# Performance work log

Hardware: AMD Instinct MI355X
Metric: run time of the kernel (lower is better)

## Reference

```python
import jax, jax.numpy as jnp
import numpy as np

N, E, NG = 4096, 8192, 256
AF, BF, H, L = 9, 4, 128, 3
LN_EPS = 1e-5


def _layernorm(x, g, b):
    mu = jnp.mean(x, axis=-1, keepdims=True)
    var = jnp.var(x, axis=-1, keepdims=True)
    return (x - mu) * jax.lax.rsqrt(var + LN_EPS) * g + b


def setup_inputs() -> dict:
    key = jax.random.key(0)
    ks = jax.random.split(key, 20)
    x = jax.random.normal(ks[0], (N, AF), dtype=jnp.float32)
    edge_index = jax.random.randint(ks[1], (2, E), 0, N, dtype=jnp.int64)
    edge_attr = jax.random.normal(ks[2], (E, BF), dtype=jnp.float32)
    batch = jnp.sort(jax.random.randint(ks[3], (N,), 0, NG, dtype=jnp.int64))
    s = lambda f: 1.0 / np.sqrt(f)
    return {
        "x": x, "edge_index": edge_index, "edge_attr": edge_attr, "batch": batch,
        "atom_w": jax.random.normal(ks[4], (AF, H), jnp.float32) * s(AF),
        "atom_b": jnp.zeros((H,), jnp.float32),
        # per-layer edge-network params, stacked over L layers
        "e1_w": jax.random.normal(ks[5], (L, BF, H), jnp.float32) * s(BF),
        "e1_b": jnp.zeros((L, H), jnp.float32),
        "e2_w": jax.random.normal(ks[6], (L, H, H * H), jnp.float32) * s(H),
        "e2_b": jnp.zeros((L, H * H), jnp.float32),
        "root_w": jax.random.normal(ks[7], (L, H, H), jnp.float32) * s(H),
        "conv_b": jnp.zeros((L, H), jnp.float32),
        "ln_g": jnp.ones((L, H), jnp.float32),
        "ln_b": jnp.zeros((L, H), jnp.float32),
        "head_w1": jax.random.normal(ks[8], (H, H // 2), jnp.float32) * s(H),
        "head_b1": jnp.zeros((H // 2,), jnp.float32),
        "head_w2": jax.random.normal(ks[9], (H // 2, 1), jnp.float32) * s(H // 2),
        "head_b2": jnp.zeros((1,), jnp.float32),
    }


def reference(x, edge_index, edge_attr, batch, atom_w, atom_b, e1_w, e1_b,
              e2_w, e2_b, root_w, conv_b, ln_g, ln_b, head_w1, head_b1,
              head_w2, head_b2):
    src, dst = edge_index[0], edge_index[1]
    h = jax.nn.relu(x @ atom_w + atom_b)  # [N, H]
    # in-degree for mean aggregation (empty -> 0 via clamp on denominator)
    deg = jax.ops.segment_sum(jnp.ones((E,), h.dtype), dst, num_segments=N)
    denom = jnp.maximum(deg, 1.0)[:, None]
    for l in range(L):
        # edge network: bond features -> per-edge HxH weight matrix
        eh = jax.nn.gelu(edge_attr @ e1_w[l] + e1_b[l], approximate=False)
        w = (eh @ e2_w[l] + e2_b[l]).reshape(E, H, H)  # [E, H, H]
        # gather source node features, per-edge matvec, scatter-mean to dst
        msg = jnp.einsum('ei,eio->eo', h[src], w)  # [E, H]
        agg = jax.ops.segment_sum(msg, dst, num_segments=N) / denom
        h_new = jax.nn.relu(agg + h @ root_w[l] + conv_b[l])
        h = _layernorm(h + h_new, ln_g[l], ln_b[l])
        # dropout: eval mode (identity)
    # global mean pool over graphs
    cnt = jnp.maximum(jax.ops.segment_sum(jnp.ones((N,), h.dtype), batch, num_segments=NG), 1.0)
    mol = jax.ops.segment_sum(h, batch, num_segments=NG) / cnt[:, None]
    hid = jax.nn.gelu(mol @ head_w1 + head_b1, approximate=False)
    logits = (hid @ head_w2 + head_b2).squeeze(-1)  # [NG]
    return logits
```

## Files before the change

kernel.cpp:

```cpp
#include <hip/hip_runtime.h>
#include <hip/hip_bf16.h>

#define N_NODES 4096
#define N_EDGES 8192
#define NGRAPH  256
#define AFEAT   9
#define BFEAT   4
#define H       128
#define NL      3
#define KS      129
#define SPLITS  4
#define TILE_E  64
#define SLICE_SH    16384
#define SLICE_BYTES 32768

typedef short short8 __attribute__((ext_vector_type(8)));
typedef float f32x4 __attribute__((ext_vector_type(4)));

__device__ __forceinline__ short f2b(float f){
    union { float f; unsigned u; } c; c.f = f;
    unsigned r = c.u + 0x7FFFu + ((c.u >> 16) & 1u);
    return (short)(r >> 16);
}
__device__ __forceinline__ float gelu_exact(float x){
    return 0.5f * x * (1.0f + erff(x * 0.70710678118654752440f));
}

__global__ void k_prep_b(const float* __restrict__ e2w, const float* __restrict__ e2b,
                         short* __restrict__ bt){
    __shared__ float ts[H][33];
    int b  = blockIdx.x;
    int o0 = (b & 3) * 32;
    int k  = (b >> 2) % KS;
    int l  = (b >> 2) / KS;
    const float* src = (k < H) ? (e2w + ((size_t)l * H + k) * (H * H))
                               : (e2b + (size_t)l * (H * H));
    for (int idx = threadIdx.x; idx < H * 32; idx += 256){
        int i = idx >> 5, op = idx & 31;
        ts[i][op] = src[i * H + o0 + op];
    }
    __syncthreads();
    short* dst = bt + (size_t)(l * KS + k) * SLICE_SH;
    for (int idx = threadIdx.x; idx < 32 * H; idx += 256){
        int j    = idx & 7;
        int quad = (idx >> 3) & 3;
        int op   = (idx >> 5) & 31;
        int ic   = idx >> 10;
        int i    = ic * 32 + quad * 8 + j;
        int o    = o0 + op;
        dst[((((o >> 4) * 4 + ic) * 64) + quad * 16 + (o & 15)) * 8 + j] = f2b(ts[i][op]);
    }
}

__global__ void k_atom(const float* __restrict__ x, const float* __restrict__ aw,
                       const float* __restrict__ ab, float* __restrict__ h,
                       short* __restrict__ hb){
    __shared__ float xs[AFEAT];
    int n = blockIdx.x, o = threadIdx.x;
    if (o < AFEAT) xs[o] = x[n * AFEAT + o];
    __syncthreads();
    float a = ab[o];
    #pragma unroll
    for (int f = 0; f < AFEAT; ++f) a += xs[f] * aw[f * H + o];
    a = fmaxf(a, 0.0f);
    h[(size_t)n * H + o]  = a;
    hb[(size_t)n * H + o] = f2b(a);
}

__global__ void k_deg(const int* __restrict__ ei, int* __restrict__ ideg){
    int e = blockIdx.x * 256 + threadIdx.x;
    if (e < N_EDGES) atomicAdd(&ideg[ei[N_EDGES + e]], 1);
}

__global__ void k_scan(const int* __restrict__ ideg, int* __restrict__ row_ptr,
                       int* __restrict__ cursor){
    __shared__ int part[256];
    int t = threadIdx.x;
    int base = t * 16;
    int loc[16]; int s = 0;
    #pragma unroll
    for (int i = 0; i < 16; ++i){ loc[i] = s; s += ideg[base + i]; }
    part[t] = s;
    __syncthreads();
    if (t == 0){
        int run = 0;
        for (int i = 0; i < 256; ++i){ int v = part[i]; part[i] = run; run += v; }
        row_ptr[N_NODES] = run;
    }
    __syncthreads();
    int off = part[t];
    #pragma unroll
    for (int i = 0; i < 16; ++i){
        row_ptr[base + i] = off + loc[i];
        cursor[base + i]  = off + loc[i];
    }
}

__global__ void k_fill(const int* __restrict__ ei, int* __restrict__ cursor,
                       int* __restrict__ eidx){
    int e = blockIdx.x * 256 + threadIdx.x;
    if (e < N_EDGES){
        int d = ei[N_EDGES + e];
        int pos = atomicAdd(&cursor[d], 1);
        eidx[pos] = e;
    }
}

__global__ void k_edge_mlp(const float* __restrict__ ea, const float* __restrict__ w1,
                           const float* __restrict__ b1, float* __restrict__ ehT){
    __shared__ float as[BFEAT];
    int e = blockIdx.x, o = threadIdx.x;
    if (o < BFEAT) as[o] = ea[e * BFEAT + o];
    __syncthreads();
    #pragma unroll
    for (int l = 0; l < NL; ++l){
        float v = b1[l * H + o];
        #pragma unroll
        for (int f = 0; f < BFEAT; ++f) v += as[f] * w1[(l * BFEAT + f) * H + o];
        v = gelu_exact(v);
        ehT[((size_t)l * KS + o) * N_EDGES + e] = v;
        if (o == 0) ehT[((size_t)l * KS + H) * N_EDGES + e] = 1.0f;
    }
}

__global__ __launch_bounds__(256, 2)
void k_msg_gemm(const short* __restrict__ bt, const float* __restrict__ ehT,
                const short* __restrict__ hb, const int* __restrict__ ei,
                float* __restrict__ parts, int l){
    __shared__ __align__(16) float ehs[33 * TILE_E];

    const int tid  = threadIdx.x;
    const int lane = tid & 63, w = tid >> 6;
    const int col  = lane & 15, quad = lane >> 4;

    const int split = blockIdx.x & 3;
    const int ohalf = (blockIdx.x >> 2) & 1;
    const int tile  = blockIdx.x >> 3;
    const int t     = ohalf * 4 + w;
    const int kbeg  = (KS * split) >> 2;
    const int kend  = (KS * (split + 1)) >> 2;
    const int kcnt  = kend - kbeg;
    const int ebase = tile * TILE_E;

    for (int idx = tid; idx < kcnt * TILE_E; idx += 256){
        int kk = idx >> 6, e = idx & 63;
        ehs[idx] = ehT[((size_t)(l * KS + kbeg + kk)) * N_EDGES + ebase + e];
    }

    short8 gf[4][4];
    #pragma unroll
    for (int m = 0; m < 4; ++m){
        int e = ebase + m * 16 + col;
        int s = ei[e];
        const char* gb = (const char*)hb + ((size_t)s * H + quad * 8) * 2;
        #pragma unroll
        for (int ic = 0; ic < 4; ++ic)
            gf[m][ic] = *(const short8*)(gb + ic * 64);
    }

    float acc[4][4];
    #pragma unroll
    for (int m = 0; m < 4; ++m)
        #pragma unroll
        for (int r = 0; r < 4; ++r) acc[m][r] = 0.0f;

    const char* bsrc = (const char*)bt + (size_t)(l * KS + kbeg) * SLICE_BYTES
                     + t * 4096 + lane * 16;

    short8 X[4], Y[4];

    auto loadB = [&](short8 (&B)[4], int kk){
        const char* p = bsrc + (size_t)kk * SLICE_BYTES;
        #pragma unroll
        for (int ic = 0; ic < 4; ++ic)
            B[ic] = *(const short8*)(p + ic * 1024);
    };
    auto computeB = [&](const short8 (&B)[4], int kk){
        __builtin_amdgcn_s_setprio(1);
        #pragma unroll
        for (int m = 0; m < 4; ++m){
            f32x4 ev = *(const f32x4*)(ehs + kk * TILE_E + m * 16 + quad * 4);
            f32x4 U = {0.0f, 0.0f, 0.0f, 0.0f};
            #pragma unroll
            for (int ic = 0; ic < 4; ++ic)
                U = __builtin_amdgcn_mfma_f32_16x16x32_bf16(gf[m][ic], B[ic], U, 0, 0, 0);
            #pragma unroll
            for (int r = 0; r < 4; ++r)
                acc[m][r] += ev[r] * U[r];
        }
        __builtin_amdgcn_s_setprio(0);
    };

    loadB(X, 0);
    __syncthreads();

    int kk = 0;
    for (; kk + 2 <= kcnt; kk += 2){
        loadB(Y, kk + 1);
        computeB(X, kk);
        if (kk + 2 < kcnt) loadB(X, kk + 2);
        computeB(Y, kk + 1);
    }
    if (kk < kcnt) computeB(X, kk);

    float* pb = parts + (size_t)split * N_EDGES * H + (size_t)ebase * H + t * 16;
    #pragma unroll
    for (int m = 0; m < 4; ++m)
        #pragma unroll
        for (int r = 0; r < 4; ++r)
            pb[(size_t)(m * 16 + quad * 4 + r) * H + col] = acc[m][r];
}

__global__ void k_node(const float* __restrict__ parts, const int* __restrict__ eidx,
                       const int* __restrict__ row_ptr,
                       const float* __restrict__ rw, const float* __restrict__ cb,
                       const float* __restrict__ lg, const float* __restrict__ lb,
                       float* __restrict__ h, short* __restrict__ hb, int l){
    __shared__ float hs[H];
    __shared__ float rsum[2], rsq[2];
    int n = blockIdx.x, o = threadIdx.x;
    float hv = h[(size_t)n * H + o];
    hs[o] = hv;
    int p0 = row_ptr[n], p1 = row_ptr[n + 1];
    float a = 0.0f;
    for (int p = p0; p < p1; ++p){
        const float* pr = parts + (size_t)eidx[p] * H + o;
        #pragma unroll
        for (int s = 0; s < SPLITS; ++s) a += pr[(size_t)s * N_EDGES * H];
    }
    int d = p1 - p0;
    a *= 1.0f / (float)(d > 0 ? d : 1);
    __syncthreads();
    float root = cb[l * H + o];
    const float* W = rw + (size_t)l * H * H;
    #pragma unroll 8
    for (int i = 0; i < H; ++i) root += hs[i] * W[i * H + o];
    float hn = fmaxf(a + root, 0.0f);
    float v  = hv + hn;
    float s = v, q = v * v;
    #pragma unroll
    for (int off = 32; off > 0; off >>= 1){
        s += __shfl_down(s, off, 64);
        q += __shfl_down(q, off, 64);
    }
    if ((o & 63) == 0){ rsum[o >> 6] = s; rsq[o >> 6] = q; }
    __syncthreads();
    float S = rsum[0] + rsum[1], Q = rsq[0] + rsq[1];
    float mean = S * (1.0f / H);
    float var  = Q * (1.0f / H) - mean * mean;
    float out  = (v - mean) * rsqrtf(var + 1e-5f) * lg[l * H + o] + lb[l * H + o];
    h[(size_t)n * H + o]  = out;
    hb[(size_t)n * H + o] = f2b(out);
}

__global__ void k_pool(const float* __restrict__ h, const int* __restrict__ batch,
                       float* __restrict__ molsum, float* __restrict__ cnt){
    int idx = blockIdx.x * 256 + threadIdx.x;
    int n = idx >> 7, o = idx & 127;
    int b = batch[n];
    atomicAdd(&molsum[b * H + o], h[idx]);
    if (o == 0) atomicAdd(&cnt[b], 1.0f);
}

__global__ void k_head(const float* __restrict__ molsum, const float* __restrict__ cnt,
                       const float* __restrict__ w1, const float* __restrict__ b1,
                       const float* __restrict__ w2, const float* __restrict__ b2,
                       float* __restrict__ out){
    __shared__ float mol[H];
    int g = blockIdx.x, t = threadIdx.x;
    float c = fmaxf(cnt[g], 1.0f);
    mol[t]      = molsum[g * H + t] / c;
    mol[t + 64] = molsum[g * H + t + 64] / c;
    __syncthreads();
    float a = b1[t];
    #pragma unroll 8
    for (int i = 0; i < H; ++i) a += mol[i] * w1[i * 64 + t];
    float hid = gelu_exact(a);
    float p = hid * w2[t];
    #pragma unroll
    for (int off = 32; off > 0; off >>= 1) p += __shfl_down(p, off, 64);
    if (t == 0) out[g] = p + b2[0];
}

extern "C" void kernel_launch(void* const* d_in, const int* in_sizes, int n_in,
                              void* d_out, int out_size, void* d_ws, size_t ws_size,
                              hipStream_t stream){
    (void)in_sizes; (void)n_in; (void)out_size; (void)ws_size;
    const float* x     = (const float*)d_in[0];
    const int*   ei    = (const int*)  d_in[1];
    const float* ea    = (const float*)d_in[2];
    const int*   batch = (const int*)  d_in[3];
    const float* aw    = (const float*)d_in[4];
    const float* ab    = (const float*)d_in[5];
    const float* e1w   = (const float*)d_in[6];
    const float* e1b   = (const float*)d_in[7];
    const float* e2w   = (const float*)d_in[8];
    const float* e2b   = (const float*)d_in[9];
    const float* rw    = (const float*)d_in[10];
    const float* cb    = (const float*)d_in[11];
    const float* lg    = (const float*)d_in[12];
    const float* lb    = (const float*)d_in[13];
    const float* hw1   = (const float*)d_in[14];
    const float* hb1   = (const float*)d_in[15];
    const float* hw2   = (const float*)d_in[16];
    const float* hb2   = (const float*)d_in[17];
    float* out = (float*)d_out;

    char* p = (char*)d_ws;
    auto carve = [&](size_t bytes){ char* r = p; p += (bytes + 255) & ~(size_t)255; return r; };
    short* bt     = (short*)carve((size_t)NL * KS * SLICE_SH * 2);
    float* h      = (float*)carve((size_t)N_NODES * H * 4);
    short* hbuf   = (short*)carve((size_t)N_NODES * H * 2);
    float* ehT    = (float*)carve((size_t)NL * KS * N_EDGES * 4);
    float* parts  = (float*)carve((size_t)SPLITS * N_EDGES * H * 4);
    int*   ideg   = (int*)  carve((size_t)N_NODES * 4);
    int*   row_ptr= (int*)  carve((size_t)(N_NODES + 1) * 4);
    int*   cursor = (int*)  carve((size_t)N_NODES * 4);
    int*   eidx   = (int*)  carve((size_t)N_EDGES * 4);
    float* molsum = (float*)carve((size_t)NGRAPH * H * 4);
    float* cnt    = (float*)carve((size_t)NGRAPH * 4);

    hipMemsetAsync(ideg, 0, (size_t)N_NODES * 4, stream);
    hipMemsetAsync(molsum, 0, (size_t)NGRAPH * H * 4, stream);
    hipMemsetAsync(cnt, 0, (size_t)NGRAPH * 4, stream);

    k_prep_b<<<NL * KS * 4, 256, 0, stream>>>(e2w, e2b, bt);
    k_atom<<<N_NODES, H, 0, stream>>>(x, aw, ab, h, hbuf);
    k_deg<<<N_EDGES / 256, 256, 0, stream>>>(ei, ideg);
    k_scan<<<1, 256, 0, stream>>>(ideg, row_ptr, cursor);
    k_fill<<<N_EDGES / 256, 256, 0, stream>>>(ei, cursor, eidx);
    k_edge_mlp<<<N_EDGES, H, 0, stream>>>(ea, e1w, e1b, ehT);

    for (int l = 0; l < NL; ++l){
        k_msg_gemm<<<(N_EDGES / TILE_E) * 2 * SPLITS, 256, 0, stream>>>(bt, ehT, hbuf, ei, parts, l);
        k_node<<<N_NODES, H, 0, stream>>>(parts, eidx, row_ptr, rw, cb, lg, lb, h, hbuf, l);
    }
    k_pool<<<N_NODES * H / 256, 256, 0, stream>>>(h, batch, molsum, cnt);
    k_head<<<NGRAPH, 64, 0, stream>>>(molsum, cnt, hw1, hb1, hw2, hb2, out);
}
```

Measured before the change: 320.5 us.

## Use three K splits with triple-buffered B loads, batch nodes, fuse pooling

The message GEMM now splits K into three equal slices of 43 instead of four uneven ones, and triple-buffers the B-fragment loads to hide more global latency. The node kernel handles four nodes per block so each root-weight load is reused across them, and the last layer folds mean pooling into it through atomics, removing the separate pool kernel. The edge MLP is relaid so each thread handles one edge for one output channel, giving coalesced ehT writes. In exchange the GEMM launches fewer blocks, uses more registers for the third buffer, and the node kernel has fewer blocks in flight.

```diff
diff --git a/kernel.cpp b/kernel.cpp
--- a/kernel.cpp
+++ b/kernel.cpp
@@ -9,8 +9,10 @@
 #define H       128
 #define NL      3
 #define KS      129
-#define SPLITS  4
+#define SPLITS  3
+#define KSPL    43
 #define TILE_E  64
+#define NPB     4
 #define SLICE_SH    16384
 #define SLICE_BYTES 32768
 
@@ -108,15 +110,16 @@
 
 __global__ void k_edge_mlp(const float* __restrict__ ea, const float* __restrict__ w1,
                            const float* __restrict__ b1, float* __restrict__ ehT){
-    __shared__ float as[BFEAT];
-    int e = blockIdx.x, o = threadIdx.x;
-    if (o < BFEAT) as[o] = ea[e * BFEAT + o];
-    __syncthreads();
+    int o = blockIdx.x >> 5;
+    int e = (blockIdx.x & 31) * 256 + threadIdx.x;
+    float4 a = *(const float4*)(ea + (size_t)e * BFEAT);
     #pragma unroll
     for (int l = 0; l < NL; ++l){
-        float v = b1[l * H + o];
-        #pragma unroll
-        for (int f = 0; f < BFEAT; ++f) v += as[f] * w1[(l * BFEAT + f) * H + o];
+        float v = b1[l * H + o]
+                + a.x * w1[(l * BFEAT + 0) * H + o]
+                + a.y * w1[(l * BFEAT + 1) * H + o]
+                + a.z * w1[(l * BFEAT + 2) * H + o]
+                + a.w * w1[(l * BFEAT + 3) * H + o];
         v = gelu_exact(v);
         ehT[((size_t)l * KS + o) * N_EDGES + e] = v;
         if (o == 0) ehT[((size_t)l * KS + H) * N_EDGES + e] = 1.0f;
@@ -127,19 +130,19 @@
 void k_msg_gemm(const short* __restrict__ bt, const float* __restrict__ ehT,
                 const short* __restrict__ hb, const int* __restrict__ ei,
                 float* __restrict__ parts, int l){
-    __shared__ __align__(16) float ehs[33 * TILE_E];
+    __shared__ __align__(16) float ehs[KSPL * TILE_E];
 
     const int tid  = threadIdx.x;
     const int lane = tid & 63, w = tid >> 6;
     const int col  = lane & 15, quad = lane >> 4;
 
-    const int split = blockIdx.x & 3;
-    const int ohalf = (blockIdx.x >> 2) & 1;
-    const int tile  = blockIdx.x >> 3;
+    const int split = blockIdx.x % 3;
+    const int rest  = blockIdx.x / 3;
+    const int ohalf = rest & 1;
+    const int tile  = rest >> 1;
     const int t     = ohalf * 4 + w;
-    const int kbeg  = (KS * split) >> 2;
-    const int kend  = (KS * (split + 1)) >> 2;
-    const int kcnt  = kend - kbeg;
+    const int kbeg  = split * KSPL;
+    const int kcnt  = KSPL;
     const int ebase = tile * TILE_E;
 
     for (int idx = tid; idx < kcnt * TILE_E; idx += 256){
@@ -167,7 +170,7 @@
     const char* bsrc = (const char*)bt + (size_t)(l * KS + kbeg) * SLICE_BYTES
                      + t * 4096 + lane * 16;
 
-    short8 X[4], Y[4];
+    short8 X[4], Y[4], Z[4];
 
     auto loadB = [&](short8 (&B)[4], int kk){
         const char* p = bsrc + (size_t)kk * SLICE_BYTES;
@@ -191,17 +194,18 @@
         __builtin_amdgcn_s_setprio(0);
     };
 
-    loadB(X, 0);
+    loadB(X, 0); loadB(Y, 1); loadB(Z, 2);
     __syncthreads();
 
     int kk = 0;
-    for (; kk + 2 <= kcnt; kk += 2){
-        loadB(Y, kk + 1);
-        computeB(X, kk);
-        if (kk + 2 < kcnt) loadB(X, kk + 2);
-        computeB(Y, kk + 1);
-    }
-    if (kk < kcnt) computeB(X, kk);
+    for (; kk + 3 < kcnt; kk += 3){
+        computeB(X, kk);     loadB(X, kk + 3);
+        computeB(Y, kk + 1); if (kk + 4 < kcnt) loadB(Y, kk + 4);
+        computeB(Z, kk + 2); if (kk + 5 < kcnt) loadB(Z, kk + 5);
+    }
+    computeB(X, kk);
+    if (kk + 1 < kcnt) computeB(Y, kk + 1);
+    if (kk + 2 < kcnt) computeB(Z, kk + 2);
 
     float* pb = parts + (size_t)split * N_EDGES * H + (size_t)ebase * H + t * 16;
     #pragma unroll
@@ -215,51 +219,73 @@
                        const int* __restrict__ row_ptr,
                        const float* __restrict__ rw, const float* __restrict__ cb,
                        const float* __restrict__ lg, const float* __restrict__ lb,
-                       float* __restrict__ h, short* __restrict__ hb, int l){
-    __shared__ float hs[H];
-    __shared__ float rsum[2], rsq[2];
-    int n = blockIdx.x, o = threadIdx.x;
-    float hv = h[(size_t)n * H + o];
-    hs[o] = hv;
-    int p0 = row_ptr[n], p1 = row_ptr[n + 1];
-    float a = 0.0f;
-    for (int p = p0; p < p1; ++p){
-        const float* pr = parts + (size_t)eidx[p] * H + o;
-        #pragma unroll
-        for (int s = 0; s < SPLITS; ++s) a += pr[(size_t)s * N_EDGES * H];
-    }
-    int d = p1 - p0;
-    a *= 1.0f / (float)(d > 0 ? d : 1);
-    __syncthreads();
-    float root = cb[l * H + o];
+                       float* __restrict__ h, short* __restrict__ hb,
+                       const int* __restrict__ batch, float* __restrict__ molsum,
+                       float* __restrict__ cnt, int l, int dolast){
+    __shared__ float hs[NPB][H];
+    __shared__ float red[NPB][2][2];
+    int n0 = blockIdx.x * NPB, o = threadIdx.x;
     const float* W = rw + (size_t)l * H * H;
+
+    float hv[NPB], root[NPB], a[NPB];
+    #pragma unroll
+    for (int m = 0; m < NPB; ++m){
+        hv[m] = h[(size_t)(n0 + m) * H + o];
+        hs[m][o] = hv[m];
+        root[m] = cb[l * H + o];
+    }
+    __syncthreads();
+
+    #pragma unroll
+    for (int m = 0; m < NPB; ++m){
+        int p0 = row_ptr[n0 + m], p1 = row_ptr[n0 + m + 1];
+        float s = 0.0f;
+        for (int p = p0; p < p1; ++p){
+            const float* pr = parts + (size_t)eidx[p] * H + o;
+            #pragma unroll
+            for (int sp = 0; sp < SPLITS; ++sp) s += pr[(size_t)sp * N_EDGES * H];
+        }
+        int d = p1 - p0;
+        a[m] = s / (float)(d > 0 ? d : 1);
+    }
+
     #pragma unroll 8
-    for (int i = 0; i < H; ++i) root += hs[i] * W[i * H + o];
-    float hn = fmaxf(a + root, 0.0f);
-    float v  = hv + hn;
-    float s = v, q = v * v;
-    #pragma unroll
-    for (int off = 32; off > 0; off >>= 1){
-        s += __shfl_down(s, off, 64);
-        q += __shfl_down(q, off, 64);
-    }
-    if ((o & 63) == 0){ rsum[o >> 6] = s; rsq[o >> 6] = q; }
-    __syncthreads();
-    float S = rsum[0] + rsum[1], Q = rsq[0] + rsq[1];
-    float mean = S * (1.0f / H);
-    float var  = Q * (1.0f / H) - mean * mean;
-    float out  = (v - mean) * rsqrtf(var + 1e-5f) * lg[l * H + o] + lb[l * H + o];
-    h[(size_t)n * H + o]  = out;
-    hb[(size_t)n * H + o] = f2b(out);
-}
-
-__global__ void k_pool(const float* __restrict__ h, const int* __restrict__ batch,
-                       float* __restrict__ molsum, float* __restrict__ cnt){
-    int idx = blockIdx.x * 256 + threadIdx.x;
-    int n = idx >> 7, o = idx & 127;
-    int b = batch[n];
-    atomicAdd(&molsum[b * H + o], h[idx]);
-    if (o == 0) atomicAdd(&cnt[b], 1.0f);
+    for (int i = 0; i < H; ++i){
+        float wv = W[i * H + o];
+        #pragma unroll
+        for (int m = 0; m < NPB; ++m) root[m] += hs[m][i] * wv;
+    }
+
+    float v[NPB];
+    #pragma unroll
+    for (int m = 0; m < NPB; ++m){
+        float hn = fmaxf(a[m] + root[m], 0.0f);
+        v[m] = hv[m] + hn;
+        float s = v[m], q = v[m] * v[m];
+        #pragma unroll
+        for (int off = 32; off > 0; off >>= 1){
+            s += __shfl_down(s, off, 64);
+            q += __shfl_down(q, off, 64);
+        }
+        if ((o & 63) == 0){ red[m][0][o >> 6] = s; red[m][1][o >> 6] = q; }
+    }
+    __syncthreads();
+    #pragma unroll
+    for (int m = 0; m < NPB; ++m){
+        float S = red[m][0][0] + red[m][0][1];
+        float Q = red[m][1][0] + red[m][1][1];
+        float mean = S * (1.0f / H);
+        float var  = Q * (1.0f / H) - mean * mean;
+        float out  = (v[m] - mean) * rsqrtf(var + 1e-5f) * lg[l * H + o] + lb[l * H + o];
+        int n = n0 + m;
+        h[(size_t)n * H + o]  = out;
+        hb[(size_t)n * H + o] = f2b(out);
+        if (dolast){
+            int b = batch[n];
+            atomicAdd(&molsum[b * H + o], out);
+            if (o == 0) atomicAdd(&cnt[b], 1.0f);
+        }
+    }
 }
 
 __global__ void k_head(const float* __restrict__ molsum, const float* __restrict__ cnt,
@@ -329,12 +355,13 @@
     k_deg<<<N_EDGES / 256, 256, 0, stream>>>(ei, ideg);
     k_scan<<<1, 256, 0, stream>>>(ideg, row_ptr, cursor);
     k_fill<<<N_EDGES / 256, 256, 0, stream>>>(ei, cursor, eidx);
-    k_edge_mlp<<<N_EDGES, H, 0, stream>>>(ea, e1w, e1b, ehT);
+    k_edge_mlp<<<H * (N_EDGES / 256), 256, 0, stream>>>(ea, e1w, e1b, ehT);
 
     for (int l = 0; l < NL; ++l){
         k_msg_gemm<<<(N_EDGES / TILE_E) * 2 * SPLITS, 256, 0, stream>>>(bt, ehT, hbuf, ei, parts, l);
-        k_node<<<N_NODES, H, 0, stream>>>(parts, eidx, row_ptr, rw, cb, lg, lb, h, hbuf, l);
-    }
-    k_pool<<<N_NODES * H / 256, 256, 0, stream>>>(h, batch, molsum, cnt);
+        k_node<<<N_NODES / NPB, H, 0, stream>>>(parts, eidx, row_ptr, rw, cb, lg, lb,
+                                                h, hbuf, batch, molsum, cnt, l,
+                                                l == NL - 1 ? 1 : 0);
+    }
     k_head<<<NGRAPH, 64, 0, stream>>>(molsum, cnt, hw1, hb1, hw2, hb2, out);
 }
```

Result: faster. 313.6 us (-2.1%).
